# Performance work log

Measured on AMD Instinct MI355X. Metric: run time of the kernel, lower is better.

## Reference

```python
import jax, jax.numpy as jnp
import numpy as np

N = 200_000            # nodes
E = 4_000_000          # edges
GCN_DIMS = [1, 20, 15, 12, 10]
NN_DIMS = [10, 32, 16, 8]
RAW = 16


def setup_inputs() -> dict:
    key = jax.random.key(0)
    ks = jax.random.split(key, 32)
    inp = {
        "x": jax.random.normal(ks[0], (N, GCN_DIMS[0]), dtype=jnp.float32),
        "edge_index": jax.random.randint(ks[1], (2, E), 0, N, dtype=jnp.int64),
    }
    ki = 2
    # GraphConv params: lin_rel (W_rel, b_rel) applied to aggregated neighbors,
    # lin_root (W_root, no bias) applied to self features.
    for i in range(4):
        fi, fo = GCN_DIMS[i], GCN_DIMS[i + 1]
        s = 1.0 / np.sqrt(fi)
        inp[f"gcn{i+1}_Wr"] = jax.random.uniform(ks[ki], (fo, fi), jnp.float32, -s, s); ki += 1
        inp[f"gcn{i+1}_b"]  = jax.random.uniform(ks[ki], (fo,),   jnp.float32, -s, s); ki += 1
        inp[f"gcn{i+1}_Wl"] = jax.random.uniform(ks[ki], (fo, fi), jnp.float32, -s, s); ki += 1
    fc_dims = NN_DIMS + [RAW]
    for i in range(4):
        fi, fo = fc_dims[i], fc_dims[i + 1]
        s = 1.0 / np.sqrt(fi)
        inp[f"fc{i+1}_W"] = jax.random.uniform(ks[ki], (fo, fi), jnp.float32, -s, s); ki += 1
        inp[f"fc{i+1}_b"] = jax.random.uniform(ks[ki], (fo,),   jnp.float32, -s, s); ki += 1
    return inp


def _graph_conv(x, src, tgt, deg_inv, Wr, b, Wl):
    # gather neighbor features, scatter-mean to targets, then two linears
    msg = x[src]                                            # [E, F]
    agg = jax.ops.segment_sum(msg, tgt, num_segments=N)     # [N, F]
    mean = agg * deg_inv                                    # [N, F]
    return mean @ Wr.T + b + x @ Wl.T                       # [N, Fo]


def reference(x, edge_index,
              gcn1_Wr, gcn1_b, gcn1_Wl, gcn2_Wr, gcn2_b, gcn2_Wl,
              gcn3_Wr, gcn3_b, gcn3_Wl, gcn4_Wr, gcn4_b, gcn4_Wl,
              fc1_W, fc1_b, fc2_W, fc2_b, fc3_W, fc3_b, fc4_W, fc4_b):
    sp = jax.nn.softplus
    src, tgt = edge_index[0], edge_index[1]
    cnt = jax.ops.segment_sum(jnp.ones((E,), x.dtype), tgt, num_segments=N)
    deg_inv = (1.0 / jnp.maximum(cnt, 1.0))[:, None]        # mean=0 for isolated nodes
    h = sp(_graph_conv(x, src, tgt, deg_inv, gcn1_Wr, gcn1_b, gcn1_Wl))
    h = sp(_graph_conv(h, src, tgt, deg_inv, gcn2_Wr, gcn2_b, gcn2_Wl))
    h = sp(_graph_conv(h, src, tgt, deg_inv, gcn3_Wr, gcn3_b, gcn3_Wl))
    h = sp(_graph_conv(h, src, tgt, deg_inv, gcn4_Wr, gcn4_b, gcn4_Wl))
    h = sp(h @ fc1_W.T + fc1_b)
    h = sp(h @ fc2_W.T + fc2_b)
    h = sp(h @ fc3_W.T + fc3_b)
    return h @ fc4_W.T + fc4_b
```

## Files before the change

kernel.cpp:

```cpp
#include <hip/hip_runtime.h>

#define NN 200000
#define NE 4000000

constexpr int BSH = 9;
constexpr int BW = 1 << BSH;
constexpr int NB2 = (NN + BW - 1) / BW;
constexpr int NWG1 = 512;
constexpr int CH = (NE + NWG1 - 1) / NWG1;
constexpr int CAP = 12288;
static_assert(NWG1 == 512, "shifts below assume 512");

__device__ __forceinline__ float softplus_f(float x) {
    return fmaxf(x, 0.0f) + log1pf(expf(-fabsf(x)));
}


__global__ __launch_bounds__(1024) void k_hist(const int* __restrict__ tgt,
                                               int* __restrict__ hist) {
    __shared__ int h[NB2];
    int w = blockIdx.x, t = threadIdx.x;
    for (int i = t; i < NB2; i += 1024) h[i] = 0;
    __syncthreads();
    int lo = w * CH, hi = min(lo + CH, NE);
    for (int e = lo + t; e < hi; e += 1024) atomicAdd(&h[tgt[e] >> BSH], 1);
    __syncthreads();
    for (int i = t; i < NB2; i += 1024) hist[w * NB2 + i] = h[i];
}

__global__ __launch_bounds__(512) void k_colscan(const int* __restrict__ hist,
                                                 int* __restrict__ loc,
                                                 int* __restrict__ bktot) {
    __shared__ int sd[512];
    int b = blockIdx.x, w = threadIdx.x;
    int v = hist[w * NB2 + b];
    sd[w] = v;
    __syncthreads();
    for (int off = 1; off < 512; off <<= 1) {
        int x = (w >= off) ? sd[w - off] : 0;
        __syncthreads();
        sd[w] += x;
        __syncthreads();
    }
    loc[b * NWG1 + w] = sd[w] - v;
    if (w == 511) bktot[b] = sd[511];
}

__global__ __launch_bounds__(512) void k_bktscan(const int* __restrict__ bktot,
                                                 int* __restrict__ bkbase) {
    __shared__ int sd[512];
    int t = threadIdx.x;
    int v = (t < NB2) ? bktot[t] : 0;
    sd[t] = v;
    __syncthreads();
    for (int off = 1; off < 512; off <<= 1) {
        int x = (t >= off) ? sd[t - off] : 0;
        __syncthreads();
        sd[t] += x;
        __syncthreads();
    }
    if (t < NB2) bkbase[t] = sd[t] - v;
    if (t == 0) bkbase[NB2] = NE;
}

__global__ __launch_bounds__(1024) void k_scatter(const int* __restrict__ ei,
                                                  const int* __restrict__ hist,
                                                  const int* __restrict__ loc,
                                                  const int* __restrict__ bkbase,
                                                  unsigned int* __restrict__ pair) {
    __shared__ int h[NB2], lc[NB2], adj[NB2];
    __shared__ int sc[512];
    __shared__ unsigned int stg[CH];
    __shared__ unsigned short stb[CH];
    int w = blockIdx.x, t = threadIdx.x;
    if (t < NB2) h[t] = hist[w * NB2 + t];
    if (t < 512) sc[t] = (t < NB2) ? hist[w * NB2 + t] : 0;
    __syncthreads();
    for (int off = 1; off < 512; off <<= 1) {
        int v = 0;
        if (t < 512 && t >= off) v = sc[t - off];
        __syncthreads();
        if (t < 512) sc[t] += v;
        __syncthreads();
    }
    if (t < NB2) {
        int lbase = sc[t] - h[t];
        lc[t] = lbase;
        adj[t] = loc[t * NWG1 + w] + bkbase[t] - lbase;
    }
    __syncthreads();
    int lo = w * CH, hi = min(lo + CH, NE);
    for (int e = lo + t; e < hi; e += 1024) {
        int s = ei[e], tg = ei[NE + e];
        int b = tg >> BSH;
        int lp = atomicAdd(&lc[b], 1);
        stg[lp] = ((unsigned int)s << BSH) | (unsigned int)(tg & (BW - 1));
        stb[lp] = (unsigned short)b;
    }
    __syncthreads();
    int n = hi - lo;
    for (int i = t; i < n; i += 1024) {
        pair[adj[stb[i]] + i] = stg[i];
    }
}

__global__ __launch_bounds__(1024) void k_bucketfill(const unsigned int* __restrict__ pair,
                                                     const int* __restrict__ bkbase,
                                                     int* __restrict__ rowptr,
                                                     float* __restrict__ dinv,
                                                     int* __restrict__ col) {
    __shared__ int nc[BW], sc[BW], cur[BW];
    __shared__ int colseg[CAP];
    int b = blockIdx.x, t = threadIdx.x;
    int lo = bkbase[b], hi = bkbase[b + 1];
    int cnt = hi - lo;
    if (t < BW) nc[t] = 0;
    __syncthreads();
    for (int e = lo + t; e < hi; e += 1024) atomicAdd(&nc[pair[e] & (BW - 1)], 1);
    __syncthreads();
    if (t < BW) sc[t] = nc[t];
    __syncthreads();
    for (int off = 1; off < BW; off <<= 1) {
        int v = 0;
        if (t < BW && t >= off) v = sc[t - off];
        __syncthreads();
        if (t < BW) sc[t] += v;
        __syncthreads();
    }
    if (t < BW) {
        int nofs = sc[t] - nc[t];
        cur[t] = nofs;
        int g = (b << BSH) + t;
        if (g < NN) {
            rowptr[g] = lo + nofs;
            dinv[g] = 1.0f / fmaxf((float)nc[t], 1.0f);
        }
    }
    if (b == NB2 - 1 && t == 0) rowptr[NN] = NE;
    __syncthreads();
    bool fast = (cnt <= CAP);
    for (int e = lo + t; e < hi; e += 1024) {
        unsigned int v = pair[e];
        int p = atomicAdd(&cur[v & (BW - 1)], 1);
        if (fast) colseg[p] = (int)(v >> BSH);
        else col[lo + p] = (int)(v >> BSH);
    }
    __syncthreads();
    if (fast) {
        for (int i = t; i < cnt; i += 1024) col[lo + i] = colseg[i];
    }
}


template <int FI, int LDI>
__device__ __forceinline__ void load_row(const float* __restrict__ p, float* v) {
    if constexpr (FI == 1) {
        v[0] = p[0];
        v[1] = 0.f; v[2] = 0.f; v[3] = 0.f;
    } else {
        constexpr int NV = (FI + 3) / 4;
        static_assert(NV * 4 <= LDI || FI == LDI, "row pad");
#pragma unroll
        for (int i = 0; i < NV; ++i) {
            float4 t = ((const float4*)p)[i];
            v[4 * i + 0] = t.x;
            v[4 * i + 1] = t.y;
            v[4 * i + 2] = t.z;
            v[4 * i + 3] = t.w;
        }
    }
}

template <int FI, int LDI, int FO, int LDO>
__global__ __launch_bounds__(256) void k_gcn(const float* __restrict__ xin,
                                             const int* __restrict__ rowptr,
                                             const int* __restrict__ col,
                                             const float* __restrict__ dinv,
                                             const float* __restrict__ Wr,
                                             const float* __restrict__ bias,
                                             const float* __restrict__ Wl,
                                             float* __restrict__ out) {
    constexpr int NV = (FI + 3) / 4, RF = NV * 4;
    constexpr int NVO = (FO + 3) / 4, RO = NVO * 4;
    static_assert(RO <= LDO, "out pad");
    __shared__ float sWr[FO * FI], sWl[FO * FI], sB[FO];
    for (int i = threadIdx.x; i < FO * FI; i += 256) {
        sWr[i] = Wr[i];
        sWl[i] = Wl[i];
    }
    if (threadIdx.x < FO) sB[threadIdx.x] = bias[threadIdx.x];
    __syncthreads();

    int n = blockIdx.x * 256 + threadIdx.x;
    if (n >= NN) return;

    float xv[RF], s[RF];
    load_row<FI, LDI>(xin + (size_t)n * LDI, xv);
#pragma unroll
    for (int f = 0; f < RF; ++f) s[f] = 0.f;

    int beg = rowptr[n], end = rowptr[n + 1];
    int j = beg;
    for (; j + 1 < end; j += 2) {
        int c0 = __ldg(&col[j]);
        int c1 = __ldg(&col[j + 1]);
        float nv0[RF], nv1[RF];
        load_row<FI, LDI>(xin + (size_t)c0 * LDI, nv0);
        load_row<FI, LDI>(xin + (size_t)c1 * LDI, nv1);
#pragma unroll
        for (int f = 0; f < RF; ++f) s[f] += nv0[f] + nv1[f];
    }
    if (j < end) {
        int c = __ldg(&col[j]);
        float nv[RF];
        load_row<FI, LDI>(xin + (size_t)c * LDI, nv);
#pragma unroll
        for (int f = 0; f < RF; ++f) s[f] += nv[f];
    }

    float di = dinv[n];
    float o_[RO];
#pragma unroll
    for (int o = 0; o < FO; ++o) {
        float aR = 0.f, aL = 0.f;
#pragma unroll
        for (int f = 0; f < FI; ++f) {
            aR = fmaf(s[f], sWr[o * FI + f], aR);
            aL = fmaf(xv[f], sWl[o * FI + f], aL);
        }
        o_[o] = softplus_f(fmaf(aR, di, sB[o]) + aL);
    }
#pragma unroll
    for (int o = FO; o < RO; ++o) o_[o] = 0.f;
#pragma unroll
    for (int i = 0; i < NVO; ++i) {
        ((float4*)(out + (size_t)n * LDO))[i] =
            make_float4(o_[4 * i], o_[4 * i + 1], o_[4 * i + 2], o_[4 * i + 3]);
    }
}


__global__ __launch_bounds__(256) void k_gcn4_fc(
    const float* __restrict__ xin,
    const int* __restrict__ rowptr, const int* __restrict__ col,
    const float* __restrict__ dinv, const float* __restrict__ Wr,
    const float* __restrict__ bias, const float* __restrict__ Wl,
    const float* __restrict__ f1W, const float* __restrict__ f1b,
    const float* __restrict__ f2W, const float* __restrict__ f2b,
    const float* __restrict__ f3W, const float* __restrict__ f3b,
    const float* __restrict__ f4W, const float* __restrict__ f4b,
    float* __restrict__ out)
{
    __shared__ float sWr[10 * 12], sWl[10 * 12], sB[10];
    __shared__ float s1W[32 * 10], s1b[32];
    __shared__ float s2W[16 * 32], s2b[16];
    __shared__ float s3W[8 * 16], s3b[8];
    __shared__ float s4W[16 * 8], s4b[16];
    for (int i = threadIdx.x; i < 120; i += 256) {
        sWr[i] = Wr[i];
        sWl[i] = Wl[i];
    }
    for (int i = threadIdx.x; i < 320; i += 256) s1W[i] = f1W[i];
    for (int i = threadIdx.x; i < 512; i += 256) s2W[i] = f2W[i];
    for (int i = threadIdx.x; i < 128; i += 256) s3W[i] = f3W[i];
    for (int i = threadIdx.x; i < 128; i += 256) s4W[i] = f4W[i];
    if (threadIdx.x < 10) sB[threadIdx.x] = bias[threadIdx.x];
    if (threadIdx.x < 32) s1b[threadIdx.x] = f1b[threadIdx.x];
    if (threadIdx.x < 16) s2b[threadIdx.x] = f2b[threadIdx.x];
    if (threadIdx.x < 8) s3b[threadIdx.x] = f3b[threadIdx.x];
    if (threadIdx.x < 16) s4b[threadIdx.x] = f4b[threadIdx.x];
    __syncthreads();

    int n = blockIdx.x * 256 + threadIdx.x;
    if (n >= NN) return;

    constexpr int FI = 12, LDI = 12;
    float xv[12], s[12];
    load_row<FI, LDI>(xin + (size_t)n * LDI, xv);
#pragma unroll
    for (int f = 0; f < 12; ++f) s[f] = 0.f;
    int beg = rowptr[n], end = rowptr[n + 1];
    int j = beg;
    for (; j + 1 < end; j += 2) {
        int c0 = __ldg(&col[j]);
        int c1 = __ldg(&col[j + 1]);
        float nv0[12], nv1[12];
        load_row<FI, LDI>(xin + (size_t)c0 * LDI, nv0);
        load_row<FI, LDI>(xin + (size_t)c1 * LDI, nv1);
#pragma unroll
        for (int f = 0; f < 12; ++f) s[f] += nv0[f] + nv1[f];
    }
    if (j < end) {
        int c = __ldg(&col[j]);
        float nv[12];
        load_row<FI, LDI>(xin + (size_t)c * LDI, nv);
#pragma unroll
        for (int f = 0; f < 12; ++f) s[f] += nv[f];
    }
    float di = dinv[n];

    float a0[10];
#pragma unroll
    for (int o = 0; o < 10; ++o) {
        float aR = 0.f, aL = 0.f;
#pragma unroll
        for (int f = 0; f < 12; ++f) {
            aR = fmaf(s[f], sWr[o * 12 + f], aR);
            aL = fmaf(xv[f], sWl[o * 12 + f], aL);
        }
        a0[o] = softplus_f(fmaf(aR, di, sB[o]) + aL);
    }

    float a1[32];
#pragma unroll
    for (int o = 0; o < 32; ++o) {
        float acc = s1b[o];
#pragma unroll
        for (int f = 0; f < 10; ++f) acc = fmaf(a0[f], s1W[o * 10 + f], acc);
        a1[o] = softplus_f(acc);
    }
    float a2[16];
#pragma unroll
    for (int o = 0; o < 16; ++o) {
        float acc = s2b[o];
#pragma unroll
        for (int f = 0; f < 32; ++f) acc = fmaf(a1[f], s2W[o * 32 + f], acc);
        a2[o] = softplus_f(acc);
    }
    float a3[8];
#pragma unroll
    for (int o = 0; o < 8; ++o) {
        float acc = s3b[o];
#pragma unroll
        for (int f = 0; f < 16; ++f) acc = fmaf(a2[f], s3W[o * 16 + f], acc);
        a3[o] = softplus_f(acc);
    }
    float a4[16];
#pragma unroll
    for (int o = 0; o < 16; ++o) {
        float acc = s4b[o];
#pragma unroll
        for (int f = 0; f < 8; ++f) acc = fmaf(a3[f], s4W[o * 8 + f], acc);
        a4[o] = acc;
    }

    float4* po = (float4*)(out + (size_t)n * 16);
#pragma unroll
    for (int i = 0; i < 4; ++i)
        po[i] = make_float4(a4[4 * i], a4[4 * i + 1], a4[4 * i + 2], a4[4 * i + 3]);
}


extern "C" void kernel_launch(void* const* d_in, const int* in_sizes, int n_in,
                              void* d_out, int out_size, void* d_ws, size_t ws_size,
                              hipStream_t stream) {
    const float* x = (const float*)d_in[0];
    const int* ei = (const int*)d_in[1];
    const float* g1Wr = (const float*)d_in[2];
    const float* g1b = (const float*)d_in[3];
    const float* g1Wl = (const float*)d_in[4];
    const float* g2Wr = (const float*)d_in[5];
    const float* g2b = (const float*)d_in[6];
    const float* g2Wl = (const float*)d_in[7];
    const float* g3Wr = (const float*)d_in[8];
    const float* g3b = (const float*)d_in[9];
    const float* g3Wl = (const float*)d_in[10];
    const float* g4Wr = (const float*)d_in[11];
    const float* g4b = (const float*)d_in[12];
    const float* g4Wl = (const float*)d_in[13];
    const float* f1W = (const float*)d_in[14];
    const float* f1b = (const float*)d_in[15];
    const float* f2W = (const float*)d_in[16];
    const float* f2b = (const float*)d_in[17];
    const float* f3W = (const float*)d_in[18];
    const float* f3b = (const float*)d_in[19];
    const float* f4W = (const float*)d_in[20];
    const float* f4b = (const float*)d_in[21];
    float* out = (float*)d_out;

    char* ws = (char*)d_ws;
    size_t off = 0;
    auto alloc = [&](size_t bytes) {
        void* p = ws + off;
        off = (off + bytes + 255) & ~(size_t)255;
        return p;
    };
    int* hist = (int*)alloc((size_t)NWG1 * NB2 * 4);
    int* loc = (int*)alloc((size_t)NB2 * NWG1 * 4);
    int* bktot = (int*)alloc((size_t)NB2 * 4);
    int* bkbase = (int*)alloc((size_t)(NB2 + 1) * 4);
    unsigned int* pair = (unsigned int*)alloc((size_t)NE * 4);
    int* rowptr = (int*)alloc((size_t)(NN + 1) * 4);
    float* dinv = (float*)alloc((size_t)NN * 4);
    int* col = (int*)alloc((size_t)NE * 4);
    float* hA = (float*)alloc((size_t)NN * 20 * 4);
    float* hB = out;

    k_hist<<<NWG1, 1024, 0, stream>>>(ei + NE, hist);
    k_colscan<<<NB2, 512, 0, stream>>>(hist, loc, bktot);
    k_bktscan<<<1, 512, 0, stream>>>(bktot, bkbase);
    k_scatter<<<NWG1, 1024, 0, stream>>>(ei, hist, loc, bkbase, pair);
    k_bucketfill<<<NB2, 1024, 0, stream>>>(pair, bkbase, rowptr, dinv, col);

    const int GB = (NN + 255) / 256;
    k_gcn<1, 1, 20, 20><<<GB, 256, 0, stream>>>(x, rowptr, col, dinv, g1Wr, g1b, g1Wl, hA);
    k_gcn<20, 20, 15, 16><<<GB, 256, 0, stream>>>(hA, rowptr, col, dinv, g2Wr, g2b, g2Wl, hB);
    k_gcn<15, 16, 12, 12><<<GB, 256, 0, stream>>>(hB, rowptr, col, dinv, g3Wr, g3b, g3Wl, hA);
    k_gcn4_fc<<<GB, 256, 0, stream>>>(hA, rowptr, col, dinv, g4Wr, g4b, g4Wl, f1W, f1b, f2W,
                                      f2b, f3W, f3b, f4W, f4b, out);
}
```

Measured before the change: 634.3 us.

## Split each node's neighbor gather across two threads with shuffle reduction

Each GCN layer kernel now assigns two threads per node, each summing alternate edges of the node's neighbor list, then combines the partial sums with a lane-pair shuffle. Blocks grow to 512 threads so each still covers 256 nodes, and only one lane of each pair writes the output. The aim is more memory-level parallelism and shorter per-thread serial chains in the latency-bound random gathers. The cost is that the dense linear, softplus and FC-chain math is now computed twice per node, and the register cap from the new launch bounds may cause spills.

```diff
diff --git a/kernel.cpp b/kernel.cpp
--- a/kernel.cpp
+++ b/kernel.cpp
@@ -171,52 +171,65 @@
     }
 }
 
+template <int FI, int LDI>
+__device__ __forceinline__ void gather_half(const float* __restrict__ xin,
+                                            const int* __restrict__ col,
+                                            int beg, int end, int half, float* s) {
+    constexpr int NV = (FI + 3) / 4, RF = NV * 4;
+#pragma unroll
+    for (int f = 0; f < RF; ++f) s[f] = 0.f;
+    int j = beg + half;
+    for (; j + 2 < end; j += 4) {
+        int c0 = __ldg(&col[j]);
+        int c1 = __ldg(&col[j + 2]);
+        float nv0[RF], nv1[RF];
+        load_row<FI, LDI>(xin + (size_t)c0 * LDI, nv0);
+        load_row<FI, LDI>(xin + (size_t)c1 * LDI, nv1);
+#pragma unroll
+        for (int f = 0; f < RF; ++f) s[f] += nv0[f] + nv1[f];
+    }
+    if (j < end) {
+        int c = __ldg(&col[j]);
+        float nv[RF];
+        load_row<FI, LDI>(xin + (size_t)c * LDI, nv);
+#pragma unroll
+        for (int f = 0; f < RF; ++f) s[f] += nv[f];
+    }
+}
+
 template <int FI, int LDI, int FO, int LDO>
-__global__ __launch_bounds__(256) void k_gcn(const float* __restrict__ xin,
-                                             const int* __restrict__ rowptr,
-                                             const int* __restrict__ col,
-                                             const float* __restrict__ dinv,
-                                             const float* __restrict__ Wr,
-                                             const float* __restrict__ bias,
-                                             const float* __restrict__ Wl,
-                                             float* __restrict__ out) {
+__global__ __launch_bounds__(512, 6) void k_gcn(const float* __restrict__ xin,
+                                                const int* __restrict__ rowptr,
+                                                const int* __restrict__ col,
+                                                const float* __restrict__ dinv,
+                                                const float* __restrict__ Wr,
+                                                const float* __restrict__ bias,
+                                                const float* __restrict__ Wl,
+                                                float* __restrict__ out) {
     constexpr int NV = (FI + 3) / 4, RF = NV * 4;
     constexpr int NVO = (FO + 3) / 4, RO = NVO * 4;
     static_assert(RO <= LDO, "out pad");
     __shared__ float sWr[FO * FI], sWl[FO * FI], sB[FO];
-    for (int i = threadIdx.x; i < FO * FI; i += 256) {
+    for (int i = threadIdx.x; i < FO * FI; i += 512) {
         sWr[i] = Wr[i];
         sWl[i] = Wl[i];
     }
     if (threadIdx.x < FO) sB[threadIdx.x] = bias[threadIdx.x];
     __syncthreads();
 
-    int n = blockIdx.x * 256 + threadIdx.x;
+    int t = threadIdx.x;
+    int n = blockIdx.x * 256 + (t >> 1);
+    int half = t & 1;
     if (n >= NN) return;
 
-    float xv[RF], s[RF];
+    float xv[RF];
     load_row<FI, LDI>(xin + (size_t)n * LDI, xv);
-#pragma unroll
-    for (int f = 0; f < RF; ++f) s[f] = 0.f;
 
     int beg = rowptr[n], end = rowptr[n + 1];
-    int j = beg;
-    for (; j + 1 < end; j += 2) {
-        int c0 = __ldg(&col[j]);
-        int c1 = __ldg(&col[j + 1]);
-        float nv0[RF], nv1[RF];
-        load_row<FI, LDI>(xin + (size_t)c0 * LDI, nv0);
-        load_row<FI, LDI>(xin + (size_t)c1 * LDI, nv1);
-#pragma unroll
-        for (int f = 0; f < RF; ++f) s[f] += nv0[f] + nv1[f];
-    }
-    if (j < end) {
-        int c = __ldg(&col[j]);
-        float nv[RF];
-        load_row<FI, LDI>(xin + (size_t)c * LDI, nv);
-#pragma unroll
-        for (int f = 0; f < RF; ++f) s[f] += nv[f];
-    }
+    float s[RF];
+    gather_half<FI, LDI>(xin, col, beg, end, half, s);
+#pragma unroll
+    for (int f = 0; f < RF; ++f) s[f] += __shfl_xor(s[f], 1);
 
     float di = dinv[n];
     float o_[RO];
@@ -232,15 +245,17 @@
     }
 #pragma unroll
     for (int o = FO; o < RO; ++o) o_[o] = 0.f;
-#pragma unroll
-    for (int i = 0; i < NVO; ++i) {
-        ((float4*)(out + (size_t)n * LDO))[i] =
-            make_float4(o_[4 * i], o_[4 * i + 1], o_[4 * i + 2], o_[4 * i + 3]);
-    }
-}
-
-
-__global__ __launch_bounds__(256) void k_gcn4_fc(
+    if (half == 0) {
+#pragma unroll
+        for (int i = 0; i < NVO; ++i) {
+            ((float4*)(out + (size_t)n * LDO))[i] =
+                make_float4(o_[4 * i], o_[4 * i + 1], o_[4 * i + 2], o_[4 * i + 3]);
+        }
+    }
+}
+
+
+__global__ __launch_bounds__(512, 6) void k_gcn4_fc(
     const float* __restrict__ xin,
     const int* __restrict__ rowptr, const int* __restrict__ col,
     const float* __restrict__ dinv, const float* __restrict__ Wr,
@@ -256,14 +271,14 @@
     __shared__ float s2W[16 * 32], s2b[16];
     __shared__ float s3W[8 * 16], s3b[8];
     __shared__ float s4W[16 * 8], s4b[16];
-    for (int i = threadIdx.x; i < 120; i += 256) {
+    for (int i = threadIdx.x; i < 120; i += 512) {
         sWr[i] = Wr[i];
         sWl[i] = Wl[i];
     }
-    for (int i = threadIdx.x; i < 320; i += 256) s1W[i] = f1W[i];
-    for (int i = threadIdx.x; i < 512; i += 256) s2W[i] = f2W[i];
-    for (int i = threadIdx.x; i < 128; i += 256) s3W[i] = f3W[i];
-    for (int i = threadIdx.x; i < 128; i += 256) s4W[i] = f4W[i];
+    for (int i = threadIdx.x; i < 320; i += 512) s1W[i] = f1W[i];
+    for (int i = threadIdx.x; i < 512; i += 512) s2W[i] = f2W[i];
+    for (int i = threadIdx.x; i < 128; i += 512) s3W[i] = f3W[i];
+    for (int i = threadIdx.x; i < 128; i += 512) s4W[i] = f4W[i];
     if (threadIdx.x < 10) sB[threadIdx.x] = bias[threadIdx.x];
     if (threadIdx.x < 32) s1b[threadIdx.x] = f1b[threadIdx.x];
     if (threadIdx.x < 16) s2b[threadIdx.x] = f2b[threadIdx.x];
@@ -271,32 +286,19 @@
     if (threadIdx.x < 16) s4b[threadIdx.x] = f4b[threadIdx.x];
     __syncthreads();
 
-    int n = blockIdx.x * 256 + threadIdx.x;
+    int t = threadIdx.x;
+    int n = blockIdx.x * 256 + (t >> 1);
+    int half = t & 1;
     if (n >= NN) return;
 
     constexpr int FI = 12, LDI = 12;
-    float xv[12], s[12];
+    float xv[12];
     load_row<FI, LDI>(xin + (size_t)n * LDI, xv);
-#pragma unroll
-    for (int f = 0; f < 12; ++f) s[f] = 0.f;
     int beg = rowptr[n], end = rowptr[n + 1];
-    int j = beg;
-    for (; j + 1 < end; j += 2) {
-        int c0 = __ldg(&col[j]);
-        int c1 = __ldg(&col[j + 1]);
-        float nv0[12], nv1[12];
-        load_row<FI, LDI>(xin + (size_t)c0 * LDI, nv0);
-        load_row<FI, LDI>(xin + (size_t)c1 * LDI, nv1);
-#pragma unroll
-        for (int f = 0; f < 12; ++f) s[f] += nv0[f] + nv1[f];
-    }
-    if (j < end) {
-        int c = __ldg(&col[j]);
-        float nv[12];
-        load_row<FI, LDI>(xin + (size_t)c * LDI, nv);
-#pragma unroll
-        for (int f = 0; f < 12; ++f) s[f] += nv[f];
-    }
+    float s[12];
+    gather_half<FI, LDI>(xin, col, beg, end, half, s);
+#pragma unroll
+    for (int f = 0; f < 12; ++f) s[f] += __shfl_xor(s[f], 1);
     float di = dinv[n];
 
     float a0[10];
@@ -344,10 +346,12 @@
         a4[o] = acc;
     }
 
-    float4* po = (float4*)(out + (size_t)n * 16);
-#pragma unroll
-    for (int i = 0; i < 4; ++i)
-        po[i] = make_float4(a4[4 * i], a4[4 * i + 1], a4[4 * i + 2], a4[4 * i + 3]);
+    if (half == 0) {
+        float4* po = (float4*)(out + (size_t)n * 16);
+#pragma unroll
+        for (int i = 0; i < 4; ++i)
+            po[i] = make_float4(a4[4 * i], a4[4 * i + 1], a4[4 * i + 2], a4[4 * i + 3]);
+    }
 }
 
 
@@ -403,9 +407,9 @@
     k_bucketfill<<<NB2, 1024, 0, stream>>>(pair, bkbase, rowptr, dinv, col);
 
     const int GB = (NN + 255) / 256;
-    k_gcn<1, 1, 20, 20><<<GB, 256, 0, stream>>>(x, rowptr, col, dinv, g1Wr, g1b, g1Wl, hA);
-    k_gcn<20, 20, 15, 16><<<GB, 256, 0, stream>>>(hA, rowptr, col, dinv, g2Wr, g2b, g2Wl, hB);
-    k_gcn<15, 16, 12, 12><<<GB, 256, 0, stream>>>(hB, rowptr, col, dinv, g3Wr, g3b, g3Wl, hA);
-    k_gcn4_fc<<<GB, 256, 0, stream>>>(hA, rowptr, col, dinv, g4Wr, g4b, g4Wl, f1W, f1b, f2W,
+    k_gcn<1, 1, 20, 20><<<GB, 512, 0, stream>>>(x, rowptr, col, dinv, g1Wr, g1b, g1Wl, hA);
+    k_gcn<20, 20, 15, 16><<<GB, 512, 0, stream>>>(hA, rowptr, col, dinv, g2Wr, g2b, g2Wl, hB);
+    k_gcn<15, 16, 12, 12><<<GB, 512, 0, stream>>>(hB, rowptr, col, dinv, g3Wr, g3b, g3Wl, hA);
+    k_gcn4_fc<<<GB, 512, 0, stream>>>(hA, rowptr, col, dinv, g4Wr, g4b, g4Wl, f1W, f1b, f2W,
                                       f2b, f3W, f3b, f4W, f4b, out);
 }
```

Result: faster. 589.2 us (-7.1%).
